# Kernel tuning notes

Hardware: AMD Instinct MI355X
Metric: run time of the kernel (lower is better)

The kernel has to match this reference:

```python
import math
import jax, jax.numpy as jnp
import numpy as np

FS = 16000          # sample rate implied by undefined global `fs` in source
NFFT = 320          # win_len == frame_len
HOP = 160           # inc
C_SOUND = 340.0
ARRAY_DIS = 0.027


def _steering(F, n_ch, angle_deg):
    # h = conj(exp(-1j*2*pi*f_k * sensor * d * sin(theta)/c)) -> exp(+1j*...)
    f_k = np.arange(F) * (FS // NFFT)                      # integer bins * 50 Hz
    delay = np.arange(n_ch) * ARRAY_DIS * np.sin(angle_deg * np.pi / 180.0) / C_SOUND
    h = np.exp(1j * 2.0 * np.pi * f_k[:, None] * delay[None, :]).astype(np.complex64)
    return jnp.asarray(h)[..., None]                       # [F, C, 1]


def _stft(x, window):
    # x: [B, C, L] float32; torch.stft defaults: center=True, reflect pad
    pad = NFFT // 2
    xp = jnp.pad(x, ((0, 0), (0, 0), (pad, pad)), mode='reflect')
    T = 1 + (xp.shape[-1] - NFFT) // HOP
    idx = jnp.arange(T)[:, None] * HOP + jnp.arange(NFFT)[None, :]
    frames = xp[:, :, idx] * window                        # [B, C, T, NFFT]
    return jnp.fft.rfft(frames, axis=-1)                   # [B, C, T, F] complex64


def _istft(S):
    # S: [B, F, T] complex; torch.istft with default (rectangular) window
    frames = jnp.fft.irfft(jnp.moveaxis(S, 1, 2), n=NFFT, axis=-1)  # [B, T, NFFT]
    B, T, _ = frames.shape
    out_len = NFFT + HOP * (T - 1)
    idx = jnp.arange(T)[:, None] * HOP + jnp.arange(NFFT)[None, :]
    out = jnp.zeros((B, out_len), frames.dtype).at[:, idx].add(frames)
    wsum = jnp.zeros((out_len,), frames.dtype).at[idx.reshape(-1)].add(1.0)
    pad = NFFT // 2
    return (out / wsum)[:, pad:-pad]


def setup_inputs() -> dict:
    key = jax.random.key(0)
    B, L, C = 8, 160000, 4
    mc_wav = jax.random.normal(key, (B, L, C), dtype=jnp.float32)
    # torch.kaiser_window(320, periodic=True, beta=6)
    window = jnp.asarray(np.kaiser(NFFT + 1, 6.0)[:NFFT].astype(np.float32))
    return {"mc_wav": mc_wav, "window": window}


def reference(mc_wav, window):
    B, L, C = mc_wav.shape
    # pre-normalize: remove DC per channel, scale by per-batch global max-abs
    x = mc_wav - jnp.mean(mc_wav, axis=1, keepdims=True)
    x = x / jnp.max(jnp.abs(x), axis=(1, 2), keepdims=True)
    x = jnp.transpose(x, (0, 2, 1))                        # [B, C, L]

    S = _stft(x, window)                                   # [B, C, T, F]
    F = S.shape[-1]
    Xs = jnp.transpose(S, (2, 0, 3, 1))                    # [T, B, F, C] frames-first
    T = Xs.shape[0]

    h1 = _steering(F, C, -40.0)                            # [F, C, 1]
    h2 = _steering(F, C, 40.0)
    eye = jnp.eye(C, dtype=S.dtype)

    def beam(invR, h, X):
        num = jnp.einsum('bfcd,fdo->bfco', invR, h)        # invR @ h  [B,F,C,1]
        den = jnp.einsum('fco,bfco->bf', h.conj(), num)    # h^H invR h
        w = num[..., 0] / den[..., None]                   # [B, F, C]
        return jnp.einsum('bfc,bfc->bf', w.conj(), X)      # w^H X

    def step(RXX, inp):
        X, first = inp                                     # X: [B, F, C]
        outer = jnp.einsum('bfc,bfd->bfcd', X, X.conj())
        RXX = jnp.where(first, outer, 0.05 * RXX + 0.95 * outer)
        tr = jnp.trace(RXX, axis1=-2, axis2=-1)[..., None, None]
        invR = jnp.linalg.inv(RXX + (tr / C) * eye)        # diag-loaded inverse
        return RXX, (beam(invR, h1, X), beam(invR, h2, X))

    RXX0 = jnp.zeros((B, F, C, C), dtype=S.dtype)
    firsts = jnp.arange(T) == 0
    _, (s1, s2) = jax.lax.scan(step, RXX0, (Xs, firsts))

    S1 = jnp.transpose(s1, (1, 2, 0))                      # [B, F, T]
    S2 = jnp.transpose(s2, (1, 2, 0))
    return _istft(S1), _istft(S2)
```

## Files before the change

### kernel.cpp

```cpp
#include <hip/hip_runtime.h>
#include <hip/hip_bf16.h>
#include <math.h>

#define BB 8
#define LL 160000
#define CC 4
#define NFFT 320
#define HOP 160
#define FB 161
#define TT 1001
#define TP 1024
#define RBLK 128
#define PI_D 3.14159265358979323846
#define NPAD 160320

#define SCH 504
#define KWARM 4

#define GM 16016
#define KSEC 352
#define LDK 704
#define KT 11

typedef __attribute__((ext_vector_type(8))) short bf16x8;
typedef __attribute__((ext_vector_type(4))) float f32x4;

__device__ __forceinline__ void ldsdma16(const short* g, short* l){
    __builtin_amdgcn_global_load_lds((const __attribute__((address_space(1))) void*)g,
                                     (__attribute__((address_space(3))) void*)l, 16, 0, 0);
}

__device__ __forceinline__ float2 cmulf(float2 a, float2 b){
    return make_float2(a.x*b.x - a.y*b.y, a.x*b.y + a.y*b.x);
}
__device__ __forceinline__ float2 cmulcj(float2 a, float2 b){
    return make_float2(a.x*b.x + a.y*b.y, a.y*b.x - a.x*b.y);
}
__device__ __forceinline__ float2 cjmul(float2 a, float2 b){
    return make_float2(a.x*b.x + a.y*b.y, a.x*b.y - a.y*b.x);
}
__device__ __forceinline__ float2 csub(float2 a, float2 b){ return make_float2(a.x-b.x, a.y-b.y); }
__device__ __forceinline__ float2 cscale(float2 a, float s){ return make_float2(a.x*s, a.y*s); }
__device__ __forceinline__ float2 cdivf(float2 a, float2 b){
    float inv = 1.0f/(b.x*b.x + b.y*b.y);
    return make_float2((a.x*b.x + a.y*b.y)*inv, (a.y*b.x - a.x*b.y)*inv);
}
__device__ __forceinline__ short bf_hi(float v){
    __hip_bfloat16 h = __float2bfloat16(v);
    short s; __builtin_memcpy(&s, &h, 2); return s;
}
__device__ __forceinline__ short bf_lo(float v){
    __hip_bfloat16 h = __float2bfloat16(v);
    float r = v - __bfloat162float(h);
    __hip_bfloat16 l = __float2bfloat16(r);
    short s; __builtin_memcpy(&s, &l, 2); return s;
}

__global__ void k_gen(const float* __restrict__ win, float* __restrict__ htab,
                      short* __restrict__ Bts, short* __restrict__ Bt){
    int gid = blockIdx.x*256 + threadIdx.x;
    if (gid < 2*FB*CC){
        int i = gid;
        int c = i & 3;
        int k = (i >> 2) % FB;
        int m = i / (FB*CC);
        double coef = 2.0*PI_D*50.0*0.027*sin(40.0*PI_D/180.0)/340.0;
        double sgn = (m == 0) ? -1.0 : 1.0;
        double ph = sgn*coef*(double)k*(double)c;
        double s, c2;
        sincos(ph, &s, &c2);
        ((float2*)htab)[i] = make_float2((float)c2, (float)s);
        return;
    }
    gid -= 2*FB*CC;
    if (gid < 384*640){
        int col = gid / 640, kk = gid % 640;
        int n = (kk >= 320) ? kk - 320 : kk;
        int sec = (kk >= 320) ? 1 : 0;
        float v = 0.f;
        if (col < 2*FB){
            int k = col >> 1;
            double th = 2.0*PI_D*(double)k*(double)n/320.0;
            double s, co; sincos(th, &s, &co);
            double tw = (col & 1) ? -s : co;
            v = (float)((double)win[n]*tw);
        }
        Bts[gid] = sec ? bf_lo(v) : bf_hi(v);
        return;
    }
    gid -= 384*640;
    if (gid < NFFT*LDK){
        int n = gid / LDK, kk = gid % LDK;
        int sec = (kk >= KSEC) ? 1 : 0;
        int kk2 = kk - (sec ? KSEC : 0);
        float v = 0.f;
        if (kk2 < 2*FB){
            int bin = kk2 >> 1;
            double c = ((bin == 0 || bin == 160) ? 1.0 : 2.0) / 320.0;
            double th = 2.0*PI_D*(double)bin*(double)n/320.0;
            double s, co; sincos(th, &s, &co);
            v = (float)((kk2 & 1) ? -c*s : c*co);
        }
        Bt[(size_t)n*LDK + kk] = sec ? bf_lo(v) : bf_hi(v);
    }
}

__global__ __launch_bounds__(256) void k_stats1(const float* __restrict__ in, float* __restrict__ part){
    __shared__ float4 s4[256];
    __shared__ float4 mn4[256];
    __shared__ float4 mx4[256];
    int b = blockIdx.x / RBLK, chunk = blockIdx.x % RBLK;
    int tid = threadIdx.x;
    const float4* p = (const float4*)(in + (size_t)b*LL*CC);
    const int per = LL / RBLK;
    int start = chunk*per;
    float4 s  = make_float4(0.f,0.f,0.f,0.f);
    float4 mn = make_float4( 3.4e38f, 3.4e38f, 3.4e38f, 3.4e38f);
    float4 mx = make_float4(-3.4e38f,-3.4e38f,-3.4e38f,-3.4e38f);
    for (int i = start + tid; i < start + per; i += 256){
        float4 v = p[i];
        s.x += v.x; s.y += v.y; s.z += v.z; s.w += v.w;
        mn.x = fminf(mn.x, v.x); mn.y = fminf(mn.y, v.y); mn.z = fminf(mn.z, v.z); mn.w = fminf(mn.w, v.w);
        mx.x = fmaxf(mx.x, v.x); mx.y = fmaxf(mx.y, v.y); mx.z = fmaxf(mx.z, v.z); mx.w = fmaxf(mx.w, v.w);
    }
    s4[tid] = s; mn4[tid] = mn; mx4[tid] = mx;
    __syncthreads();
    for (int st = 128; st >= 1; st >>= 1){
        if (tid < st){
            float4 a = s4[tid], c = s4[tid+st];
            s4[tid] = make_float4(a.x+c.x, a.y+c.y, a.z+c.z, a.w+c.w);
            float4 d = mn4[tid], e = mn4[tid+st];
            mn4[tid] = make_float4(fminf(d.x,e.x), fminf(d.y,e.y), fminf(d.z,e.z), fminf(d.w,e.w));
            float4 f = mx4[tid], g = mx4[tid+st];
            mx4[tid] = make_float4(fmaxf(f.x,g.x), fmaxf(f.y,g.y), fmaxf(f.z,g.z), fmaxf(f.w,g.w));
        }
        __syncthreads();
    }
    if (tid == 0){
        float* dst = part + (size_t)(b*RBLK + chunk)*12;
        float4 a = s4[0], d = mn4[0], f = mx4[0];
        dst[0]=a.x; dst[1]=a.y; dst[2]=a.z; dst[3]=a.w;
        dst[4]=d.x; dst[5]=d.y; dst[6]=d.z; dst[7]=d.w;
        dst[8]=f.x; dst[9]=f.y; dst[10]=f.z; dst[11]=f.w;
    }
}

__global__ __launch_bounds__(128) void k_stats2(const float* __restrict__ part,
                                                float* __restrict__ mean, float* __restrict__ invmax){
    __shared__ float4 s4[128];
    __shared__ float4 mn4[128];
    __shared__ float4 mx4[128];
    int b = blockIdx.x, tid = threadIdx.x;
    const float* src = part + (size_t)(b*RBLK + tid)*12;
    s4[tid]  = make_float4(src[0], src[1], src[2], src[3]);
    mn4[tid] = make_float4(src[4], src[5], src[6], src[7]);
    mx4[tid] = make_float4(src[8], src[9], src[10], src[11]);
    __syncthreads();
    for (int st = 64; st >= 1; st >>= 1){
        if (tid < st){
            float4 a = s4[tid], c = s4[tid+st];
            s4[tid] = make_float4(a.x+c.x, a.y+c.y, a.z+c.z, a.w+c.w);
            float4 d = mn4[tid], e = mn4[tid+st];
            mn4[tid] = make_float4(fminf(d.x,e.x), fminf(d.y,e.y), fminf(d.z,e.z), fminf(d.w,e.w));
            float4 f = mx4[tid], g = mx4[tid+st];
            mx4[tid] = make_float4(fmaxf(f.x,g.x), fmaxf(f.y,g.y), fmaxf(f.z,g.z), fmaxf(f.w,g.w));
        }
        __syncthreads();
    }
    if (tid == 0){
        float4 sum = s4[0], mn = mn4[0], mx = mx4[0];
        float m0 = sum.x*(1.0f/LL), m1 = sum.y*(1.0f/LL), m2 = sum.z*(1.0f/LL), m3 = sum.w*(1.0f/LL);
        mean[b*4+0]=m0; mean[b*4+1]=m1; mean[b*4+2]=m2; mean[b*4+3]=m3;
        float a0 = fmaxf(mx.x - m0, m0 - mn.x);
        float a1 = fmaxf(mx.y - m1, m1 - mn.y);
        float a2 = fmaxf(mx.z - m2, m2 - mn.z);
        float a3 = fmaxf(mx.w - m3, m3 - mn.w);
        invmax[b] = 1.0f / fmaxf(fmaxf(a0, a1), fmaxf(a2, a3));
    }
}

__global__ __launch_bounds__(256) void k_anorm(const float* __restrict__ in,
        const float* __restrict__ mean, const float* __restrict__ invmax,
        short* __restrict__ Ahi, short* __restrict__ Alo){
    int gid = blockIdx.x*256 + threadIdx.x;
    if (gid >= BB*(NPAD/8)) return;
    int p8 = gid % (NPAD/8);
    int b  = gid / (NPAD/8);
    float4 mc = *(const float4*)&mean[b*4];
    float iv = invmax[b];
    const float4* px = (const float4*)(in + (size_t)b*LL*CC);
    bf16x8 h0{}, h1{}, h2{}, h3{}, l0{}, l1{}, l2{}, l3{};
    #pragma unroll
    for (int j = 0; j < 8; ++j){
        int p = p8*8 + j - 160;
        int m2 = p < 0 ? -p : (p >= LL ? 2*LL - 2 - p : p);
        float4 v = px[m2];
        float v0 = (v.x - mc.x)*iv, v1 = (v.y - mc.y)*iv;
        float v2 = (v.z - mc.z)*iv, v3 = (v.w - mc.w)*iv;
        h0[j] = bf_hi(v0); l0[j] = bf_lo(v0);
        h1[j] = bf_hi(v1); l1[j] = bf_lo(v1);
        h2[j] = bf_hi(v2); l2[j] = bf_lo(v2);
        h3[j] = bf_hi(v3); l3[j] = bf_lo(v3);
    }
    size_t o = (size_t)(b*4)*NPAD + (size_t)p8*8;
    *(bf16x8*)&Ahi[o]          = h0;  *(bf16x8*)&Alo[o]          = l0;
    *(bf16x8*)&Ahi[o +   NPAD] = h1;  *(bf16x8*)&Alo[o +   NPAD] = l1;
    *(bf16x8*)&Ahi[o + 2*NPAD] = h2;  *(bf16x8*)&Alo[o + 2*NPAD] = l2;
    *(bf16x8*)&Ahi[o + 3*NPAD] = h3;  *(bf16x8*)&Alo[o + 3*NPAD] = l3;
}

__global__ __launch_bounds__(512, 4) void k_gstft(const short* __restrict__ Ahi, const short* __restrict__ Alo,
        const short* __restrict__ Bts, float* __restrict__ S){
    __shared__ short stage[32768];
    int tid = threadIdx.x;
    int row0 = blockIdx.x*128;
    int col0 = blockIdx.y*128;
    int b  = row0 >> 12;
    int t0 = (row0 & 4095) >> 2;
    int wave = tid >> 6, lane = tid & 63;
    int wm = wave >> 1, wn = wave & 1;
    int l15 = lane & 15, quad = lane >> 4;
    int rowS  = wave*16 + (lane >> 2);
    int chunk = (lane & 3) ^ ((lane >> 3) & 3);
    int tls = t0 + (rowS >> 2); if (tls >= TT) tls = TT - 1;
    size_t gao = (size_t)(b*4 + (rowS & 3))*NPAD + (size_t)tls*160 + chunk*8;
    const short* gAh = Ahi + gao;
    const short* gAl = Alo + gao;
    const short* gB  = Bts + (size_t)(col0 + rowS)*640 + chunk*8;
    short* lA = stage + wave*512;
    int sw  = (l15 >> 1) & 3;
    int c0r = (quad ^ sw) * 8;
    int ra0 = (wm*32 + l15)*32 + c0r;
    int rb0 = (wn*64 + l15)*32 + c0r;
    f32x4 c00 = {0.f,0.f,0.f,0.f}, c01 = c00, c02 = c00, c03 = c00;
    f32x4 c10 = c00, c11 = c00, c12 = c00, c13 = c00;

    #define STG(kt_, off_) do{ \
        ldsdma16(gAh + (kt_)*32,       lA + (off_));         \
        ldsdma16(gAl + (kt_)*32,       lA + (off_) + 4096);  \
        ldsdma16(gB  + (kt_)*32,       lA + (off_) + 8192);  \
        ldsdma16(gB  + (kt_)*32 + 320, lA + (off_) + 12288); \
    }while(0)

    STG(0, 0);
    STG(1, 16384);
    #pragma unroll
    for (int kt = 0; kt < 10; ++kt){
        int offc = (kt & 1) ? 16384 : 0;
        if (kt < 9) asm volatile("s_waitcnt vmcnt(4)" ::: "memory");
        else        asm volatile("s_waitcnt vmcnt(0)" ::: "memory");
        __builtin_amdgcn_s_barrier();
        bf16x8 a0h = *(bf16x8*)&stage[offc + ra0];
        bf16x8 a1h = *(bf16x8*)&stage[offc + ra0 + 512];
        bf16x8 a0l = *(bf16x8*)&stage[offc + 4096 + ra0];
        bf16x8 a1l = *(bf16x8*)&stage[offc + 4096 + ra0 + 512];
        bf16x8 b0h = *(bf16x8*)&stage[offc + 8192 + rb0];
        bf16x8 b1h = *(bf16x8*)&stage[offc + 8192 + rb0 + 512];
        bf16x8 b2h = *(bf16x8*)&stage[offc + 8192 + rb0 + 1024];
        bf16x8 b3h = *(bf16x8*)&stage[offc + 8192 + rb0 + 1536];
        bf16x8 b0l = *(bf16x8*)&stage[offc + 12288 + rb0];
        bf16x8 b1l = *(bf16x8*)&stage[offc + 12288 + rb0 + 512];
        bf16x8 b2l = *(bf16x8*)&stage[offc + 12288 + rb0 + 1024];
        bf16x8 b3l = *(bf16x8*)&stage[offc + 12288 + rb0 + 1536];
        asm volatile("s_waitcnt lgkmcnt(0)" ::: "memory");
        __builtin_amdgcn_sched_barrier(0);
        __builtin_amdgcn_s_barrier();
        if (kt < 8) STG(kt+2, offc);
        c00 = __builtin_amdgcn_mfma_f32_16x16x32_bf16(a0h, b0h, c00, 0, 0, 0);
        c01 = __builtin_amdgcn_mfma_f32_16x16x32_bf16(a0h, b1h, c01, 0, 0, 0);
        c02 = __builtin_amdgcn_mfma_f32_16x16x32_bf16(a0h, b2h, c02, 0, 0, 0);
        c03 = __builtin_amdgcn_mfma_f32_16x16x32_bf16(a0h, b3h, c03, 0, 0, 0);
        c10 = __builtin_amdgcn_mfma_f32_16x16x32_bf16(a1h, b0h, c10, 0, 0, 0);
        c11 = __builtin_amdgcn_mfma_f32_16x16x32_bf16(a1h, b1h, c11, 0, 0, 0);
        c12 = __builtin_amdgcn_mfma_f32_16x16x32_bf16(a1h, b2h, c12, 0, 0, 0);
        c13 = __builtin_amdgcn_mfma_f32_16x16x32_bf16(a1h, b3h, c13, 0, 0, 0);
        c00 = __builtin_amdgcn_mfma_f32_16x16x32_bf16(a0l, b0h, c00, 0, 0, 0);
        c01 = __builtin_amdgcn_mfma_f32_16x16x32_bf16(a0l, b1h, c01, 0, 0, 0);
        c02 = __builtin_amdgcn_mfma_f32_16x16x32_bf16(a0l, b2h, c02, 0, 0, 0);
        c03 = __builtin_amdgcn_mfma_f32_16x16x32_bf16(a0l, b3h, c03, 0, 0, 0);
        c10 = __builtin_amdgcn_mfma_f32_16x16x32_bf16(a1l, b0h, c10, 0, 0, 0);
        c11 = __builtin_amdgcn_mfma_f32_16x16x32_bf16(a1l, b1h, c11, 0, 0, 0);
        c12 = __builtin_amdgcn_mfma_f32_16x16x32_bf16(a1l, b2h, c12, 0, 0, 0);
        c13 = __builtin_amdgcn_mfma_f32_16x16x32_bf16(a1l, b3h, c13, 0, 0, 0);
        c00 = __builtin_amdgcn_mfma_f32_16x16x32_bf16(a0h, b0l, c00, 0, 0, 0);
        c01 = __builtin_amdgcn_mfma_f32_16x16x32_bf16(a0h, b1l, c01, 0, 0, 0);
        c02 = __builtin_amdgcn_mfma_f32_16x16x32_bf16(a0h, b2l, c02, 0, 0, 0);
        c03 = __builtin_amdgcn_mfma_f32_16x16x32_bf16(a0h, b3l, c03, 0, 0, 0);
        c10 = __builtin_amdgcn_mfma_f32_16x16x32_bf16(a1h, b0l, c10, 0, 0, 0);
        c11 = __builtin_amdgcn_mfma_f32_16x16x32_bf16(a1h, b1l, c11, 0, 0, 0);
        c12 = __builtin_amdgcn_mfma_f32_16x16x32_bf16(a1h, b2l, c12, 0, 0, 0);
        c13 = __builtin_amdgcn_mfma_f32_16x16x32_bf16(a1h, b3l, c13, 0, 0, 0);
    }
    #undef STG
    int tq  = t0 + wm*8 + quad;
    int kgb = (col0 >> 1) + wn*32 + (l15 >> 1);
    int h   = l15 & 1;
    float4* S4 = (float4*)S;
    #define EPI(cf, i_, j_) do{ \
        int t = tq + 4*(i_); \
        int kg = kgb + 8*(j_); \
        if (t < TT && kg < FB){ \
            float p0 = __shfl_xor(cf[0], 1); \
            float p1 = __shfl_xor(cf[1], 1); \
            float p2 = __shfl_xor(cf[2], 1); \
            float p3 = __shfl_xor(cf[3], 1); \
            float4 v = h ? make_float4(p2, cf[2], p3, cf[3]) \
                         : make_float4(cf[0], p0, cf[1], p1); \
            S4[((size_t)((b*FB + kg)*2 + h))*TT + t] = v; \
        } \
    }while(0)
    EPI(c00, 0, 0); EPI(c01, 0, 1); EPI(c02, 0, 2); EPI(c03, 0, 3);
    EPI(c10, 1, 0); EPI(c11, 1, 1); EPI(c12, 1, 2); EPI(c13, 1, 3);
    #undef EPI
}

#define UPD(first) do{ \
    float aa = (first) ? 0.f : 0.05f; float wg = (first) ? 1.f : 0.95f; \
    float y0x=wg*x0.x, y0y=wg*x0.y, y1x=wg*x1.x, y1y=wg*x1.y; \
    float y2x=wg*x2.x, y2y=wg*x2.y, y3x=wg*x3.x, y3y=wg*x3.y; \
    d0 = aa*d0 + y0x*x0.x + y0y*x0.y; \
    d1 = aa*d1 + y1x*x1.x + y1y*x1.y; \
    d2 = aa*d2 + y2x*x2.x + y2y*x2.y; \
    d3 = aa*d3 + y3x*x3.x + y3y*x3.y; \
    r10.x = aa*r10.x + y1x*x0.x + y1y*x0.y;  r10.y = aa*r10.y + y1y*x0.x - y1x*x0.y; \
    r20.x = aa*r20.x + y2x*x0.x + y2y*x0.y;  r20.y = aa*r20.y + y2y*x0.x - y2x*x0.y; \
    r30.x = aa*r30.x + y3x*x0.x + y3y*x0.y;  r30.y = aa*r30.y + y3y*x0.x - y3x*x0.y; \
    r21.x = aa*r21.x + y2x*x1.x + y2y*x1.y;  r21.y = aa*r21.y + y2y*x1.x - y2x*x1.y; \
    r31.x = aa*r31.x + y3x*x1.x + y3y*x1.y;  r31.y = aa*r31.y + y3y*x1.x - y3x*x1.y; \
    r32.x = aa*r32.x + y3x*x2.x + y3y*x2.y;  r32.y = aa*r32.y + y3y*x2.x - y3x*x2.y; \
}while(0)

#define UPDQ do{ \
    d0 = 0.05f*d0 + x0.x*x0.x + x0.y*x0.y; \
    d1 = 0.05f*d1 + x1.x*x1.x + x1.y*x1.y; \
    d2 = 0.05f*d2 + x2.x*x2.x + x2.y*x2.y; \
    d3 = 0.05f*d3 + x3.x*x3.x + x3.y*x3.y; \
    r10.x = 0.05f*r10.x + x1.x*x0.x + x1.y*x0.y;  r10.y = 0.05f*r10.y + x1.y*x0.x - x1.x*x0.y; \
    r20.x = 0.05f*r20.x + x2.x*x0.x + x2.y*x0.y;  r20.y = 0.05f*r20.y + x2.y*x0.x - x2.x*x0.y; \
    r30.x = 0.05f*r30.x + x3.x*x0.x + x3.y*x0.y;  r30.y = 0.05f*r30.y + x3.y*x0.x - x3.x*x0.y; \
    r21.x = 0.05f*r21.x + x2.x*x1.x + x2.y*x1.y;  r21.y = 0.05f*r21.y + x2.y*x1.x - x2.x*x1.y; \
    r31.x = 0.05f*r31.x + x3.x*x1.x + x3.y*x1.y;  r31.y = 0.05f*r31.y + x3.y*x1.x - x3.x*x1.y; \
    r32.x = 0.05f*r32.x + x3.x*x2.x + x3.y*x2.y;  r32.y = 0.05f*r32.y + x3.y*x2.x - x3.x*x2.y; \
}while(0)

__global__ __launch_bounds__(512) void k_scan(const float* __restrict__ S, const float* __restrict__ htab,
                      float* __restrict__ S1, float* __restrict__ S2){
    __shared__ float4 tile[1008];
    int bid = blockIdx.x;
    int half = bid & 1;
    int bf = bid >> 1;
    int f  = bf % FB;
    int tid = threadIdx.x;
    int tbase = half*SCH;
    int te  = tbase + SCH; if (te > TT) te = TT;
    int nst = 2*(te - tbase);
    const float4* P0 = (const float4*)S + (size_t)(bf*2)*TT;
    const float4* P1 = P0 + TT;
    for (int i = tid; i < nst; i += 512){
        int tt = tbase + (i >> 1);
        tile[i ^ ((i>>4)&7)] = (i & 1) ? P1[tt] : P0[tt];
    }
    __syncthreads();
    int t0 = tbase + tid;
    bool act = (tid < SCH) && (t0 < TT);
    if (act){
        const float2* hp = (const float2*)htab;
        float2 ha0 = hp[f*4+0], ha1 = hp[f*4+1], ha2 = hp[f*4+2], ha3 = hp[f*4+3];
        float2 hb0 = hp[(FB+f)*4+0], hb1 = hp[(FB+f)*4+1], hb2 = hp[(FB+f)*4+2], hb3 = hp[(FB+f)*4+3];
        float d0=0,d1=0,d2=0,d3=0;
        float2 r10={0,0}, r20={0,0}, r30={0,0}, r21={0,0}, r31={0,0}, r32={0,0};
        float2 x0, x1, x2, x3;
        #define LOADX(tau_) do{ float4 v0_, v1_; \
            if ((tau_) >= tbase){ int i0_ = 2*((tau_) - tbase); \
                v0_ = tile[i0_ ^ ((i0_>>4)&7)]; v1_ = tile[(i0_+1) ^ ((i0_>>4)&7)]; } \
            else { v0_ = P0[tau_]; v1_ = P1[tau_]; } \
            x0 = make_float2(v0_.x, v0_.y); x1 = make_float2(v0_.z, v0_.w); \
            x2 = make_float2(v1_.x, v1_.y); x3 = make_float2(v1_.z, v1_.w); \
        }while(0)
        if (t0 >= KWARM + 1){
            #pragma unroll
            for (int u = 0; u <= KWARM; ++u){ LOADX(t0 - KWARM + u); UPDQ; }
        } else {
            for (int tau = 0; tau <= t0; ++tau){ LOADX(tau); UPD(tau == 0); }
        }
        #undef LOADX
        {
            float trc = d0 + d1 + d2 + d3;
            float lam = trc * 0.25f;
            float e0 = d0 + lam, e1 = d1 + lam, e2 = d2 + lam, e3 = d3 + lam;
            float detP = e0*e1 - (r10.x*r10.x + r10.y*r10.y);
            float2 w00 = csub(cscale(r20, e1), cmulf(r10, r21));
            float2 w01 = csub(cscale(r30, e1), cmulf(r10, r31));
            float2 w10 = csub(cscale(r21, e0), cjmul(r10, r20));
            float2 w11 = csub(cscale(r31, e0), cjmul(r10, r30));
            float2 va = cjmul(r30, w00), vb = cjmul(r31, w10);
            float2 V10 = make_float2(va.x + vb.x, -(va.y + vb.y));
            float reV00 = r20.x*w00.x + r20.y*w00.y + r21.x*w10.x + r21.y*w10.y;
            float reV11 = r30.x*w01.x + r30.y*w01.y + r31.x*w11.x + r31.y*w11.y;
            float t00 = detP*e2 - reV00;
            float t11 = detP*e3 - reV11;
            float2 t10 = csub(cscale(r32, detP), V10);
            float detT = t00*t11 - (t10.x*t10.x + t10.y*t10.y);
            float2* S1g = (float2*)S1 + (size_t)bf*TT;
            float2* S2g = (float2*)S2 + (size_t)bf*TT;
            #pragma unroll
            for (int m = 0; m < 2; ++m){
                float2 h0 = m ? hb0 : ha0;
                float2 h1 = m ? hb1 : ha1;
                float2 h2 = m ? hb2 : ha2;
                float2 h3 = m ? hb3 : ha3;
                float2 g0 = csub(cscale(h0, e1), cjmul(r10, h1));
                float2 g1 = csub(cscale(h1, e0), cmulf(r10, h0));
                float2 ta = cmulf(r20, g0), tb = cmulf(r21, g1);
                float2 hh0 = make_float2(detP*h2.x - ta.x - tb.x, detP*h2.y - ta.y - tb.y);
                ta = cmulf(r30, g0); tb = cmulf(r31, g1);
                float2 hh1 = make_float2(detP*h3.x - ta.x - tb.x, detP*h3.y - ta.y - tb.y);
                float2 y20 = csub(cscale(hh0, t11), cjmul(t10, hh1));
                float2 y21 = csub(cscale(hh1, t00), cmulf(t10, hh0));
                float2 u20 = cscale(y20, detP), u21 = cscale(y21, detP);
                ta = cmulcj(y20, r20); tb = cmulcj(y21, r30);
                float2 q0 = make_float2(detT*h0.x - ta.x - tb.x, detT*h0.y - ta.y - tb.y);
                ta = cmulcj(y20, r21); tb = cmulcj(y21, r31);
                float2 q1 = make_float2(detT*h1.x - ta.x - tb.x, detT*h1.y - ta.y - tb.y);
                float2 u10 = csub(cscale(q0, e1), cjmul(r10, q1));
                float2 u11 = csub(cscale(q1, e0), cmulf(r10, q0));
                float2 den = cjmul(h0, u10), tmp;
                tmp = cjmul(h1, u11); den.x += tmp.x; den.y += tmp.y;
                tmp = cjmul(h2, u20); den.x += tmp.x; den.y += tmp.y;
                tmp = cjmul(h3, u21); den.x += tmp.x; den.y += tmp.y;
                float2 num = cjmul(u10, x0);
                tmp = cjmul(u11, x1); num.x += tmp.x; num.y += tmp.y;
                tmp = cjmul(u20, x2); num.x += tmp.x; num.y += tmp.y;
                tmp = cjmul(u21, x3); num.x += tmp.x; num.y += tmp.y;
                float2 s = cdivf(num, make_float2(den.x, -den.y));
                if (m) S2g[t0] = s; else S1g[t0] = s;
            }
        }
    }
}

__global__ __launch_bounds__(256) void k_pack(const float* __restrict__ S1, const float* __restrict__ S2,
                                              short* __restrict__ A){
    __shared__ short tile[32*708];
    int bid = blockIdx.x;
    int tb = bid & 31, rb = bid >> 5;
    int t0 = tb*32;
    int beam = rb >> 3, b = rb & 7;
    const float2* Sp = (const float2*)(beam ? S2 : S1) + (size_t)b*FB*TT;
    int tid = threadIdx.x;
    for (int idx = tid; idx < 32*176; idx += 256){
        int bin = idx >> 5, tq = idx & 31;
        int t = t0 + tq;
        float2 s = make_float2(0.f, 0.f);
        if (bin < FB && t < TT) s = Sp[(size_t)bin*TT + t];
        int c0 = 2*bin;
        tile[tq*708 + c0]            = bf_hi(s.x);
        tile[tq*708 + c0 + 1]        = bf_hi(s.y);
        tile[tq*708 + KSEC + c0]     = bf_lo(s.x);
        tile[tq*708 + KSEC + c0 + 1] = bf_lo(s.y);
    }
    __syncthreads();
    for (int idx = tid; idx < 32*176; idx += 256){
        int tq = idx / 176, k4 = idx % 176;
        int t = t0 + tq;
        if (t < TT)
            *(short4*)&A[(size_t)(rb*TT + t)*LDK + k4*4] = *(short4*)&tile[tq*708 + k4*4];
    }
}

__global__ __launch_bounds__(512, 4) void k_gemm(const short* __restrict__ A, const short* __restrict__ Bt,
                                                 float* __restrict__ C){
    __shared__ short sb2[16384];
    int tid = threadIdx.x;
    int row0 = blockIdx.x * 128;
    int col0 = blockIdx.y * 128;
    int wave = tid >> 6, lane = tid & 63;
    int wm = wave >> 1, wn = wave & 1;
    int l15 = lane & 15, quad = lane >> 4;
    bool wlive = (col0 + wn*64) < NFFT;
    int rowS  = wave*16 + (lane >> 2);
    int chunk = (lane & 3) ^ ((lane >> 3) & 3);
    int grS = row0 + rowS; if (grS >= GM) grS = GM - 1;
    int grB = col0 + rowS; if (grB >= NFFT) grB = NFFT - 1;
    const short* gA = A  + (size_t)grS*LDK + chunk*8;
    const short* gB = Bt + (size_t)grB*LDK + chunk*8;
    short* lA = sb2 + wave*512;
    int sw  = (l15 >> 1) & 3;
    int c0r = (quad ^ sw) * 8;
    int ra0 = (wm*32 + l15)*32 + c0r;
    int rb0 = (wn*64 + l15)*32 + c0r;
    f32x4 c00 = {0.f,0.f,0.f,0.f}, c01 = c00, c02 = c00, c03 = c00;
    f32x4 c10 = c00, c11 = c00, c12 = c00, c13 = c00;

    #define KOF(s_, ka_, kb_) { int sg_ = ((s_) >= 22) ? 2 : ((s_) >= 11) ? 1 : 0; \
        int kt_ = (s_) - sg_*11; \
        ka_ = ((sg_ == 1) ? KSEC : 0) + kt_*32; \
        kb_ = ((sg_ == 2) ? KSEC : 0) + kt_*32; }
    #define STG2(s_, off_) do{ int ka_, kb_; KOF(s_, ka_, kb_); \
        ldsdma16(gA + ka_, lA + (off_));        \
        ldsdma16(gB + kb_, lA + (off_) + 4096); \
    }while(0)

    STG2(0, 0);
    STG2(1, 8192);
    #pragma unroll
    for (int s = 0; s < 33; ++s){
        int offc = (s & 1) ? 8192 : 0;
        if (s < 32) asm volatile("s_waitcnt vmcnt(2)" ::: "memory");
        else        asm volatile("s_waitcnt vmcnt(0)" ::: "memory");
        __builtin_amdgcn_s_barrier();
        bf16x8 a0{}, a1{}, b0{}, b1{}, b2{}, b3{};
        if (wlive){
            a0 = *(bf16x8*)&sb2[offc + ra0];
            a1 = *(bf16x8*)&sb2[offc + ra0 + 512];
            b0 = *(bf16x8*)&sb2[offc + 4096 + rb0];
            b1 = *(bf16x8*)&sb2[offc + 4096 + rb0 + 512];
            b2 = *(bf16x8*)&sb2[offc + 4096 + rb0 + 1024];
            b3 = *(bf16x8*)&sb2[offc + 4096 + rb0 + 1536];
            asm volatile("s_waitcnt lgkmcnt(0)" ::: "memory");
            __builtin_amdgcn_sched_barrier(0);
        }
        __builtin_amdgcn_s_barrier();
        if (s < 31) STG2(s+2, offc);
        if (wlive){
            c00 = __builtin_amdgcn_mfma_f32_16x16x32_bf16(a0, b0, c00, 0, 0, 0);
            c01 = __builtin_amdgcn_mfma_f32_16x16x32_bf16(a0, b1, c01, 0, 0, 0);
            c02 = __builtin_amdgcn_mfma_f32_16x16x32_bf16(a0, b2, c02, 0, 0, 0);
            c03 = __builtin_amdgcn_mfma_f32_16x16x32_bf16(a0, b3, c03, 0, 0, 0);
            c10 = __builtin_amdgcn_mfma_f32_16x16x32_bf16(a1, b0, c10, 0, 0, 0);
            c11 = __builtin_amdgcn_mfma_f32_16x16x32_bf16(a1, b1, c11, 0, 0, 0);
            c12 = __builtin_amdgcn_mfma_f32_16x16x32_bf16(a1, b2, c12, 0, 0, 0);
            c13 = __builtin_amdgcn_mfma_f32_16x16x32_bf16(a1, b3, c13, 0, 0, 0);
        }
    }
    #undef STG2
    #undef KOF
    if (wlive){
        #pragma unroll
        for (int r = 0; r < 4; ++r){
            int orow0 = row0 + wm*32 + quad*4 + r;
            int oc = col0 + wn*64 + l15;
            if (orow0 < GM){
                if (oc      < NFFT) C[(size_t)orow0*NFFT + oc]      = c00[r];
                if (oc + 16 < NFFT) C[(size_t)orow0*NFFT + oc + 16] = c01[r];
                if (oc + 32 < NFFT) C[(size_t)orow0*NFFT + oc + 32] = c02[r];
                if (oc + 48 < NFFT) C[(size_t)orow0*NFFT + oc + 48] = c03[r];
            }
            if (orow0 + 16 < GM){
                if (oc      < NFFT) C[(size_t)(orow0+16)*NFFT + oc]      = c10[r];
                if (oc + 16 < NFFT) C[(size_t)(orow0+16)*NFFT + oc + 16] = c11[r];
                if (oc + 32 < NFFT) C[(size_t)(orow0+16)*NFFT + oc + 32] = c12[r];
                if (oc + 48 < NFFT) C[(size_t)(orow0+16)*NFFT + oc + 48] = c13[r];
            }
        }
    }
}

__global__ __launch_bounds__(256) void k_ola(const float* __restrict__ frames, float* __restrict__ out){
    int gid = blockIdx.x*256 + threadIdx.x;
    if (gid >= 2*BB*(LL/4)) return;
    int o4 = (gid % (LL/4))*4;
    int rb = gid / (LL/4);
    int i  = o4 + HOP;
    int t1 = i / HOP;
    int r  = i - t1*HOP;
    const float4* fb = (const float4*)(frames + (size_t)rb*TT*NFFT);
    float4 a = fb[(t1*NFFT + r) >> 2];
    float4 b = fb[((t1-1)*NFFT + r + HOP) >> 2];
    ((float4*)out)[gid] = make_float4(0.5f*(a.x+b.x), 0.5f*(a.y+b.y), 0.5f*(a.z+b.z), 0.5f*(a.w+b.w));
}

extern "C" void kernel_launch(void* const* d_in, const int* in_sizes, int n_in,
                              void* d_out, int out_size, void* d_ws, size_t ws_size,
                              hipStream_t stream){
    const float* in  = (const float*)d_in[0];
    const float* win = (const float*)d_in[1];
    float* ws = (float*)d_ws;
    float* mean   = ws;
    float* invmax = ws + 32;
    float* htab   = ws + 48;
    float* S1     = ws + 3072;
    size_t nS1 = (size_t)2*BB*FB*TT;
    float* S2 = S1 + nS1;
    float* S  = S2 + nS1;
    float* part = S1;
    short* Ahi = (short*)S1;
    short* Alo = Ahi + (size_t)BB*CC*NPAD;
    short* Bts = (short*)d_out;
    short* Bt  = (short*)((float*)d_out + 131072);
    short* A  = (short*)S;
    float* frames = S1;

    int ngen = 2*FB*CC + 384*640 + NFFT*LDK;
    k_gen<<<dim3((ngen + 255)/256), dim3(256), 0, stream>>>(win, htab, Bts, Bt);
    k_stats1<<<dim3(BB*RBLK), dim3(256), 0, stream>>>(in, part);
    k_stats2<<<dim3(BB), dim3(128), 0, stream>>>(part, mean, invmax);
    k_anorm<<<dim3((BB*(NPAD/8) + 255)/256), dim3(256), 0, stream>>>(in, mean, invmax, Ahi, Alo);
    k_gstft<<<dim3(BB*TP*CC/128, 3), dim3(512), 0, stream>>>(Ahi, Alo, Bts, S);
    k_scan<<<dim3(2*BB*FB), dim3(512), 0, stream>>>(S, htab, S1, S2);
    k_pack<<<dim3(512), dim3(256), 0, stream>>>(S1, S2, A);
    k_gemm<<<dim3((GM + 127)/128, (NFFT + 127)/128), dim3(512), 0, stream>>>(A, Bt, frames);
    k_ola<<<dim3((2*BB*(LL/4) + 255)/256), dim3(256), 0, stream>>>(frames, (float*)d_out);
}
```

Baseline: 194.8 us.

## Skip padded STFT columns, merge scan halves, triple-buffer iSTFT GEMM

Three independent changes. The STFT GEMM now skips LDS loads and MFMAs for 16-column subtiles that lie past the 322 real output columns. The beamforming scan uses one block per (batch, frequency) with each thread handling two consecutive frames, sharing the windowed warm-up and halving block count. The iSTFT GEMM moves from double to triple LDS buffering, so the next stage's DMA is issued before compute and one barrier per step is removed, at the cost of 50% more shared memory per block.

```diff
diff --git a/kernel.cpp b/kernel.cpp
--- a/kernel.cpp
+++ b/kernel.cpp
@@ -14,7 +14,6 @@
 #define PI_D 3.14159265358979323846
 #define NPAD 160320
 
-#define SCH 504
 #define KWARM 4
 
 #define GM 16016
@@ -220,6 +219,10 @@
     int wave = tid >> 6, lane = tid & 63;
     int wm = wave >> 1, wn = wave & 1;
     int l15 = lane & 15, quad = lane >> 4;
+    int colb = col0 + wn*64;
+    bool bl1 = (colb + 16) < 2*FB;
+    bool bl2 = (colb + 32) < 2*FB;
+    bool bl3 = (colb + 48) < 2*FB;
     int rowS  = wave*16 + (lane >> 2);
     int chunk = (lane & 3) ^ ((lane >> 3) & 3);
     int tls = t0 + (rowS >> 2); if (tls >= TT) tls = TT - 1;
@@ -255,41 +258,48 @@
         bf16x8 a0l = *(bf16x8*)&stage[offc + 4096 + ra0];
         bf16x8 a1l = *(bf16x8*)&stage[offc + 4096 + ra0 + 512];
         bf16x8 b0h = *(bf16x8*)&stage[offc + 8192 + rb0];
-        bf16x8 b1h = *(bf16x8*)&stage[offc + 8192 + rb0 + 512];
-        bf16x8 b2h = *(bf16x8*)&stage[offc + 8192 + rb0 + 1024];
-        bf16x8 b3h = *(bf16x8*)&stage[offc + 8192 + rb0 + 1536];
         bf16x8 b0l = *(bf16x8*)&stage[offc + 12288 + rb0];
-        bf16x8 b1l = *(bf16x8*)&stage[offc + 12288 + rb0 + 512];
-        bf16x8 b2l = *(bf16x8*)&stage[offc + 12288 + rb0 + 1024];
-        bf16x8 b3l = *(bf16x8*)&stage[offc + 12288 + rb0 + 1536];
+        bf16x8 b1h{}, b2h{}, b3h{}, b1l{}, b2l{}, b3l{};
+        if (bl1){ b1h = *(bf16x8*)&stage[offc + 8192 + rb0 + 512];
+                  b1l = *(bf16x8*)&stage[offc + 12288 + rb0 + 512]; }
+        if (bl2){ b2h = *(bf16x8*)&stage[offc + 8192 + rb0 + 1024];
+                  b2l = *(bf16x8*)&stage[offc + 12288 + rb0 + 1024]; }
+        if (bl3){ b3h = *(bf16x8*)&stage[offc + 8192 + rb0 + 1536];
+                  b3l = *(bf16x8*)&stage[offc + 12288 + rb0 + 1536]; }
         asm volatile("s_waitcnt lgkmcnt(0)" ::: "memory");
         __builtin_amdgcn_sched_barrier(0);
         __builtin_amdgcn_s_barrier();
         if (kt < 8) STG(kt+2, offc);
         c00 = __builtin_amdgcn_mfma_f32_16x16x32_bf16(a0h, b0h, c00, 0, 0, 0);
-        c01 = __builtin_amdgcn_mfma_f32_16x16x32_bf16(a0h, b1h, c01, 0, 0, 0);
-        c02 = __builtin_amdgcn_mfma_f32_16x16x32_bf16(a0h, b2h, c02, 0, 0, 0);
-        c03 = __builtin_amdgcn_mfma_f32_16x16x32_bf16(a0h, b3h, c03, 0, 0, 0);
+        c00 = __builtin_amdgcn_mfma_f32_16x16x32_bf16(a0l, b0h, c00, 0, 0, 0);
+        c00 = __builtin_amdgcn_mfma_f32_16x16x32_bf16(a0h, b0l, c00, 0, 0, 0);
         c10 = __builtin_amdgcn_mfma_f32_16x16x32_bf16(a1h, b0h, c10, 0, 0, 0);
-        c11 = __builtin_amdgcn_mfma_f32_16x16x32_bf16(a1h, b1h, c11, 0, 0, 0);
-        c12 = __builtin_amdgcn_mfma_f32_16x16x32_bf16(a1h, b2h, c12, 0, 0, 0);
-        c13 = __builtin_amdgcn_mfma_f32_16x16x32_bf16(a1h, b3h, c13, 0, 0, 0);
-        c00 = __builtin_amdgcn_mfma_f32_16x16x32_bf16(a0l, b0h, c00, 0, 0, 0);
-        c01 = __builtin_amdgcn_mfma_f32_16x16x32_bf16(a0l, b1h, c01, 0, 0, 0);
-        c02 = __builtin_amdgcn_mfma_f32_16x16x32_bf16(a0l, b2h, c02, 0, 0, 0);
-        c03 = __builtin_amdgcn_mfma_f32_16x16x32_bf16(a0l, b3h, c03, 0, 0, 0);
         c10 = __builtin_amdgcn_mfma_f32_16x16x32_bf16(a1l, b0h, c10, 0, 0, 0);
-        c11 = __builtin_amdgcn_mfma_f32_16x16x32_bf16(a1l, b1h, c11, 0, 0, 0);
-        c12 = __builtin_amdgcn_mfma_f32_16x16x32_bf16(a1l, b2h, c12, 0, 0, 0);
-        c13 = __builtin_amdgcn_mfma_f32_16x16x32_bf16(a1l, b3h, c13, 0, 0, 0);
-        c00 = __builtin_amdgcn_mfma_f32_16x16x32_bf16(a0h, b0l, c00, 0, 0, 0);
-        c01 = __builtin_amdgcn_mfma_f32_16x16x32_bf16(a0h, b1l, c01, 0, 0, 0);
-        c02 = __builtin_amdgcn_mfma_f32_16x16x32_bf16(a0h, b2l, c02, 0, 0, 0);
-        c03 = __builtin_amdgcn_mfma_f32_16x16x32_bf16(a0h, b3l, c03, 0, 0, 0);
         c10 = __builtin_amdgcn_mfma_f32_16x16x32_bf16(a1h, b0l, c10, 0, 0, 0);
-        c11 = __builtin_amdgcn_mfma_f32_16x16x32_bf16(a1h, b1l, c11, 0, 0, 0);
-        c12 = __builtin_amdgcn_mfma_f32_16x16x32_bf16(a1h, b2l, c12, 0, 0, 0);
-        c13 = __builtin_amdgcn_mfma_f32_16x16x32_bf16(a1h, b3l, c13, 0, 0, 0);
+        if (bl1){
+            c01 = __builtin_amdgcn_mfma_f32_16x16x32_bf16(a0h, b1h, c01, 0, 0, 0);
+            c01 = __builtin_amdgcn_mfma_f32_16x16x32_bf16(a0l, b1h, c01, 0, 0, 0);
+            c01 = __builtin_amdgcn_mfma_f32_16x16x32_bf16(a0h, b1l, c01, 0, 0, 0);
+            c11 = __builtin_amdgcn_mfma_f32_16x16x32_bf16(a1h, b1h, c11, 0, 0, 0);
+            c11 = __builtin_amdgcn_mfma_f32_16x16x32_bf16(a1l, b1h, c11, 0, 0, 0);
+            c11 = __builtin_amdgcn_mfma_f32_16x16x32_bf16(a1h, b1l, c11, 0, 0, 0);
+        }
+        if (bl2){
+            c02 = __builtin_amdgcn_mfma_f32_16x16x32_bf16(a0h, b2h, c02, 0, 0, 0);
+            c02 = __builtin_amdgcn_mfma_f32_16x16x32_bf16(a0l, b2h, c02, 0, 0, 0);
+            c02 = __builtin_amdgcn_mfma_f32_16x16x32_bf16(a0h, b2l, c02, 0, 0, 0);
+            c12 = __builtin_amdgcn_mfma_f32_16x16x32_bf16(a1h, b2h, c12, 0, 0, 0);
+            c12 = __builtin_amdgcn_mfma_f32_16x16x32_bf16(a1l, b2h, c12, 0, 0, 0);
+            c12 = __builtin_amdgcn_mfma_f32_16x16x32_bf16(a1h, b2l, c12, 0, 0, 0);
+        }
+        if (bl3){
+            c03 = __builtin_amdgcn_mfma_f32_16x16x32_bf16(a0h, b3h, c03, 0, 0, 0);
+            c03 = __builtin_amdgcn_mfma_f32_16x16x32_bf16(a0l, b3h, c03, 0, 0, 0);
+            c03 = __builtin_amdgcn_mfma_f32_16x16x32_bf16(a0h, b3l, c03, 0, 0, 0);
+            c13 = __builtin_amdgcn_mfma_f32_16x16x32_bf16(a1h, b3h, c13, 0, 0, 0);
+            c13 = __builtin_amdgcn_mfma_f32_16x16x32_bf16(a1l, b3h, c13, 0, 0, 0);
+            c13 = __builtin_amdgcn_mfma_f32_16x16x32_bf16(a1h, b3l, c13, 0, 0, 0);
+        }
     }
     #undef STG
     int tq  = t0 + wm*8 + quad;
@@ -345,46 +355,47 @@
 
 __global__ __launch_bounds__(512) void k_scan(const float* __restrict__ S, const float* __restrict__ htab,
                       float* __restrict__ S1, float* __restrict__ S2){
-    __shared__ float4 tile[1008];
-    int bid = blockIdx.x;
-    int half = bid & 1;
-    int bf = bid >> 1;
+    __shared__ float4 tile[2016];
+    int bf = blockIdx.x;
     int f  = bf % FB;
     int tid = threadIdx.x;
-    int tbase = half*SCH;
-    int te  = tbase + SCH; if (te > TT) te = TT;
-    int nst = 2*(te - tbase);
     const float4* P0 = (const float4*)S + (size_t)(bf*2)*TT;
     const float4* P1 = P0 + TT;
-    for (int i = tid; i < nst; i += 512){
-        int tt = tbase + (i >> 1);
+    for (int i = tid; i < 2*TT; i += 512){
+        int tt = i >> 1;
         tile[i ^ ((i>>4)&7)] = (i & 1) ? P1[tt] : P0[tt];
     }
     __syncthreads();
-    int t0 = tbase + tid;
-    bool act = (tid < SCH) && (t0 < TT);
-    if (act){
+    int t0 = tid*2;
+    if (t0 < TT){
         const float2* hp = (const float2*)htab;
         float2 ha0 = hp[f*4+0], ha1 = hp[f*4+1], ha2 = hp[f*4+2], ha3 = hp[f*4+3];
         float2 hb0 = hp[(FB+f)*4+0], hb1 = hp[(FB+f)*4+1], hb2 = hp[(FB+f)*4+2], hb3 = hp[(FB+f)*4+3];
         float d0=0,d1=0,d2=0,d3=0;
         float2 r10={0,0}, r20={0,0}, r30={0,0}, r21={0,0}, r31={0,0}, r32={0,0};
         float2 x0, x1, x2, x3;
-        #define LOADX(tau_) do{ float4 v0_, v1_; \
-            if ((tau_) >= tbase){ int i0_ = 2*((tau_) - tbase); \
-                v0_ = tile[i0_ ^ ((i0_>>4)&7)]; v1_ = tile[(i0_+1) ^ ((i0_>>4)&7)]; } \
-            else { v0_ = P0[tau_]; v1_ = P1[tau_]; } \
+        #define LOADX(tau_) do{ int i0_ = 2*(tau_); \
+            float4 v0_ = tile[i0_ ^ ((i0_>>4)&7)]; \
+            float4 v1_ = tile[(i0_+1) ^ (((i0_+1)>>4)&7)]; \
             x0 = make_float2(v0_.x, v0_.y); x1 = make_float2(v0_.z, v0_.w); \
             x2 = make_float2(v1_.x, v1_.y); x3 = make_float2(v1_.z, v1_.w); \
         }while(0)
-        if (t0 >= KWARM + 1){
+        bool qform = (t0 >= KWARM + 1);
+        int ts = t0 - KWARM; if (ts < 0) ts = 0;
+        if (qform){
             #pragma unroll
-            for (int u = 0; u <= KWARM; ++u){ LOADX(t0 - KWARM + u); UPDQ; }
+            for (int u = 0; u < KWARM; ++u){ LOADX(ts + u); UPDQ; }
         } else {
-            for (int tau = 0; tau <= t0; ++tau){ LOADX(tau); UPD(tau == 0); }
-        }
-        #undef LOADX
-        {
+            for (int tau = 0; tau < t0; ++tau){ LOADX(tau); UPD(tau == 0); }
+        }
+        float2* S1g = (float2*)S1 + (size_t)bf*TT;
+        float2* S2g = (float2*)S2 + (size_t)bf*TT;
+        #pragma unroll
+        for (int j = 0; j < 2; ++j){
+            int t = t0 + j;
+            if (t >= TT) break;
+            LOADX(t);
+            if (qform) UPDQ; else UPD(t == 0);
             float trc = d0 + d1 + d2 + d3;
             float lam = trc * 0.25f;
             float e0 = d0 + lam, e1 = d1 + lam, e2 = d2 + lam, e3 = d3 + lam;
@@ -401,8 +412,6 @@
             float t11 = detP*e3 - reV11;
             float2 t10 = csub(cscale(r32, detP), V10);
             float detT = t00*t11 - (t10.x*t10.x + t10.y*t10.y);
-            float2* S1g = (float2*)S1 + (size_t)bf*TT;
-            float2* S2g = (float2*)S2 + (size_t)bf*TT;
             #pragma unroll
             for (int m = 0; m < 2; ++m){
                 float2 h0 = m ? hb0 : ha0;
@@ -433,9 +442,10 @@
                 tmp = cjmul(u20, x2); num.x += tmp.x; num.y += tmp.y;
                 tmp = cjmul(u21, x3); num.x += tmp.x; num.y += tmp.y;
                 float2 s = cdivf(num, make_float2(den.x, -den.y));
-                if (m) S2g[t0] = s; else S1g[t0] = s;
+                if (m) S2g[t] = s; else S1g[t] = s;
             }
         }
+        #undef LOADX
     }
 }
 
@@ -470,7 +480,7 @@
 
 __global__ __launch_bounds__(512, 4) void k_gemm(const short* __restrict__ A, const short* __restrict__ Bt,
                                                  float* __restrict__ C){
-    __shared__ short sb2[16384];
+    __shared__ short sb2[24576];
     int tid = threadIdx.x;
     int row0 = blockIdx.x * 128;
     int col0 = blockIdx.y * 128;
@@ -505,10 +515,11 @@
     STG2(1, 8192);
     #pragma unroll
     for (int s = 0; s < 33; ++s){
-        int offc = (s & 1) ? 8192 : 0;
+        int offc = (s % 3) * 8192;
         if (s < 32) asm volatile("s_waitcnt vmcnt(2)" ::: "memory");
         else        asm volatile("s_waitcnt vmcnt(0)" ::: "memory");
         __builtin_amdgcn_s_barrier();
+        if (s < 31) STG2(s+2, ((s+2) % 3) * 8192);
         bf16x8 a0{}, a1{}, b0{}, b1{}, b2{}, b3{};
         if (wlive){
             a0 = *(bf16x8*)&sb2[offc + ra0];
@@ -519,10 +530,6 @@
             b3 = *(bf16x8*)&sb2[offc + 4096 + rb0 + 1536];
             asm volatile("s_waitcnt lgkmcnt(0)" ::: "memory");
             __builtin_amdgcn_sched_barrier(0);
-        }
-        __builtin_amdgcn_s_barrier();
-        if (s < 31) STG2(s+2, offc);
-        if (wlive){
             c00 = __builtin_amdgcn_mfma_f32_16x16x32_bf16(a0, b0, c00, 0, 0, 0);
             c01 = __builtin_amdgcn_mfma_f32_16x16x32_bf16(a0, b1, c01, 0, 0, 0);
             c02 = __builtin_amdgcn_mfma_f32_16x16x32_bf16(a0, b2, c02, 0, 0, 0);
@@ -597,7 +604,7 @@
     k_stats2<<<dim3(BB), dim3(128), 0, stream>>>(part, mean, invmax);
     k_anorm<<<dim3((BB*(NPAD/8) + 255)/256), dim3(256), 0, stream>>>(in, mean, invmax, Ahi, Alo);
     k_gstft<<<dim3(BB*TP*CC/128, 3), dim3(512), 0, stream>>>(Ahi, Alo, Bts, S);
-    k_scan<<<dim3(2*BB*FB), dim3(512), 0, stream>>>(S, htab, S1, S2);
+    k_scan<<<dim3(BB*FB), dim3(512), 0, stream>>>(S, htab, S1, S2);
     k_pack<<<dim3(512), dim3(256), 0, stream>>>(S1, S2, A);
     k_gemm<<<dim3((GM + 127)/128, (NFFT + 127)/128), dim3(512), 0, stream>>>(A, Bt, frames);
     k_ola<<<dim3((2*BB*(LL/4) + 255)/256), dim3(256), 0, stream>>>(frames, (float*)d_out);
```

New measurement: 192.4 us. Within noise of the previous version (-1.2%).
